# Kernel tuning notes

Hardware: AMD Instinct MI355X
Metric: run time of the kernel (lower is better)

Reference implementation:

```python
import jax, jax.numpy as jnp
import numpy as np

ALPHA = 1.5
EPS = 1e-5
N_BISECT = 30

BSZ, NFIELD, NFEAT, NEMB, DK, NHID, MLP_NHID, NOUT = 2048, 100, 100000, 64, 64, 256, 1024, 1


def _entmax_bisect(x):
    """alpha-entmax (alpha=1.5) along last axis via bisection on tau."""
    x = x * (ALPHA - 1.0)
    mx = jnp.max(x, axis=-1, keepdims=True)
    d = x.shape[-1]
    tau_lo = mx - 1.0
    tau_hi = mx - (1.0 / d) ** (ALPHA - 1.0)
    inv_am1 = 1.0 / (ALPHA - 1.0)  # = 2.0 for alpha=1.5

    def p_of(tau):
        return jnp.maximum(x - tau, 0.0) ** inv_am1

    dm0 = tau_hi - tau_lo

    def body(i, carry):
        tau_lo, dm = carry
        dm = dm * 0.5
        tau_m = tau_lo + dm
        f_m = jnp.sum(p_of(tau_m), axis=-1, keepdims=True) - 1.0
        tau_lo = jnp.where(f_m >= 0, tau_m, tau_lo)
        return (tau_lo, dm)

    tau_lo, dm = jax.lax.fori_loop(0, N_BISECT, body, (tau_lo, dm0))
    p = p_of(tau_lo)
    return p / jnp.sum(p, axis=-1, keepdims=True)


@jax.custom_vjp
def entmax(x):
    return _entmax_bisect(x)

def _entmax_fwd(x):
    p = _entmax_bisect(x)
    return p, p

def _entmax_bwd(p, g):
    # exact entmax jacobian-vector product (as in entmax library)
    gppr = jnp.where(p > 0, p ** (2.0 - ALPHA), 0.0)
    dx = g * gppr
    q = jnp.sum(dx, axis=-1, keepdims=True) / jnp.sum(gppr, axis=-1, keepdims=True)
    return (dx - q * gppr,)

entmax.defvjp(_entmax_fwd, _entmax_bwd)


def _bn(x, gamma, beta, axes, ch_shape):
    mean = jnp.mean(x, axis=axes, keepdims=True)
    var = jnp.var(x, axis=axes, keepdims=True)
    return gamma.reshape(ch_shape) * (x - mean) / jnp.sqrt(var + EPS) + beta.reshape(ch_shape)


def setup_inputs() -> dict:
    key = jax.random.key(0)
    ks = jax.random.split(key, 12)
    inp = {
        "ids": jax.random.randint(ks[0], (BSZ, NFIELD), 0, NFEAT),
        "values": jax.random.uniform(ks[1], (BSZ, NFIELD), dtype=jnp.float32),
        "emb_table": jax.random.normal(ks[2], (NFEAT, NEMB), dtype=jnp.float32) * 0.01,
        "w_bilinear": jax.random.normal(ks[3], (DK, NEMB), dtype=jnp.float32) * (1.0 / np.sqrt(NEMB)),
        "query": jax.random.normal(ks[4], (NHID, DK), dtype=jnp.float32) * (1.414 / np.sqrt(NHID + DK)),
        "att_values": jax.random.normal(ks[5], (NHID, NFIELD), dtype=jnp.float32) * 0.01,
        "bn_gamma": jnp.ones((NHID,), jnp.float32),
        "bn_beta": jnp.zeros((NHID,), jnp.float32),
        "mlp_w0": jax.random.normal(ks[6], (MLP_NHID, NHID * NEMB), dtype=jnp.float32) * (1.0 / np.sqrt(NHID * NEMB)),
        "mlp_b0": jnp.zeros((MLP_NHID,), jnp.float32),
        "mlp_g0": jnp.ones((MLP_NHID,), jnp.float32),
        "mlp_be0": jnp.zeros((MLP_NHID,), jnp.float32),
        "mlp_w1": jax.random.normal(ks[7], (MLP_NHID, MLP_NHID), dtype=jnp.float32) * (1.0 / np.sqrt(MLP_NHID)),
        "mlp_b1": jnp.zeros((MLP_NHID,), jnp.float32),
        "mlp_g1": jnp.ones((MLP_NHID,), jnp.float32),
        "mlp_be1": jnp.zeros((MLP_NHID,), jnp.float32),
        "out_w": jax.random.normal(ks[8], (NOUT, MLP_NHID), dtype=jnp.float32) * (1.0 / np.sqrt(MLP_NHID)),
        "out_b": jnp.zeros((NOUT,), jnp.float32),
    }
    return inp


def reference(ids, values, emb_table, w_bilinear, query, att_values, bn_gamma, bn_beta,
              mlp_w0, mlp_b0, mlp_g0, mlp_be0, mlp_w1, mlp_b1, mlp_g1, mlp_be1, out_w, out_b):
    v = jnp.clip(values, 0.001, 1.0)                        # [b,f]
    emb = emb_table[ids] * v[..., None]                     # [b,f,e]
    keys = jnp.einsum('bfe,ke->bfk', emb, w_bilinear)       # [b,f,dk]
    gates = jnp.einsum('bfk,ok->bof', keys, query) * (DK ** -0.5)  # [b,o,f]
    sparse_gates = entmax(gates)                            # [b,o,f]
    arm_w = sparse_gates * att_values[None]                 # [b,o,f]
    arm = jnp.exp(jnp.einsum('bfe,bof->boe', emb, arm_w))   # [b,o,e]
    arm = _bn(arm, bn_gamma, bn_beta, axes=(0, 2), ch_shape=(1, -1, 1))
    h = arm.reshape(arm.shape[0], -1)                       # [b, o*e]
    h = jax.nn.relu(_bn(h @ mlp_w0.T + mlp_b0, mlp_g0, mlp_be0, axes=(0,), ch_shape=(1, -1)))
    h = jax.nn.relu(_bn(h @ mlp_w1.T + mlp_b1, mlp_g1, mlp_be1, axes=(0,), ch_shape=(1, -1)))
    y = h @ out_w.T + out_b                                 # [b,1]
    return y.squeeze(-1)
```

## Files before the change

kernel.cpp:

```cpp
#include <hip/hip_runtime.h>

typedef unsigned short u16;
typedef __attribute__((ext_vector_type(8))) short bf16x8;
typedef __attribute__((ext_vector_type(8))) unsigned short u16x8;
typedef __attribute__((ext_vector_type(4))) float f32x4;

__device__ __forceinline__ u16 f2bf(float f) {
  unsigned u = __builtin_bit_cast(unsigned, f);
  u += 0x7fffu + ((u >> 16) & 1u);
  return (u16)(u >> 16);
}
__device__ __forceinline__ float bf2f(u16 h) {
  unsigned u = ((unsigned)h) << 16;
  return __builtin_bit_cast(float, u);
}

#define NB 2048
#define NF 100
#define NE 64
#define NO 256
#define OCH 64
#define EMB_ST 72
#define EMBT_ST 136
#define GAW_ST 136

#define GLOAD16(gsrc, ldst)                                                        \
  __builtin_amdgcn_global_load_lds(                                                \
      (const __attribute__((address_space(1))) unsigned int*)(gsrc),               \
      (__attribute__((address_space(3))) unsigned int*)(ldst), 16, 0, 0)

__global__ void k_prep(const float* __restrict__ wb, const float* __restrict__ q,
                       u16* __restrict__ mt, const float* __restrict__ w1,
                       u16* __restrict__ w1bf) {
  if (blockIdx.x < 64) {
    int idx = blockIdx.x * 256 + threadIdx.x;
    int o = idx >> 6, e = idx & 63;
    float s = 0.f;
    for (int k = 0; k < 64; ++k) s = fmaf(q[o * 64 + k], wb[k * 64 + e], s);
    mt[idx] = f2bf(s * 0.0625f);
  } else {
    int i4 = ((blockIdx.x - 64) * 256 + threadIdx.x) * 4;
    float4 v = *(const float4*)(w1 + i4);
    ushort4 o;
    o.x = f2bf(v.x); o.y = f2bf(v.y); o.z = f2bf(v.z); o.w = f2bf(v.w);
    *(ushort4*)(w1bf + i4) = o;
  }
}

__global__ void k_cvt_w0s(const float* __restrict__ in, const float* __restrict__ scl,
                          u16* __restrict__ out) {
  size_t i4 = ((size_t)blockIdx.x * 256 + threadIdx.x) * 4;
  int o = (int)((i4 >> 6) & 255);
  float sc = scl[o];
  float4 v = *(const float4*)(in + i4);
  ushort4 u;
  u.x = f2bf(v.x * sc); u.y = f2bf(v.y * sc);
  u.z = f2bf(v.z * sc); u.w = f2bf(v.w * sc);
  *(ushort4*)(out + i4) = u;
}

__global__ __launch_bounds__(256) void k_mega(
    const int* __restrict__ ids, const float* __restrict__ vals,
    const float* __restrict__ etab, const u16* __restrict__ mt,
    const float* __restrict__ att, u16* __restrict__ tbuf,
    float* __restrict__ pstatB) {
  __shared__ u16 s_emb[112][EMB_ST];
  __shared__ u16 s_embT[64][EMBT_ST];
  __shared__ u16 s_gaw[64][GAW_ST];
  __shared__ float s_rs[64];
  __shared__ float s_ps[256][2];

  const int tid = threadIdx.x;
  const int lane = tid & 63;
  const int wid = tid >> 6;
  const int b = blockIdx.x;

  for (int f = wid; f < NF; f += 4) {
    int id = ids[b * NF + f];
    float v = vals[b * NF + f];
    v = fminf(fmaxf(v, 0.001f), 1.0f);
    float ev = etab[(size_t)id * NE + lane] * v;
    u16 bf = f2bf(ev);
    s_emb[f][lane] = bf;
    s_embT[lane][f] = bf;
  }
  for (int i = tid; i < 12 * EMB_ST; i += 256) s_emb[100 + i / EMB_ST][i % EMB_ST] = 0;
  for (int i = tid; i < 64 * 36; i += 256) s_embT[i / 36][100 + i % 36] = 0;
  for (int i = tid; i < 64 * 24; i += 256) s_gaw[i / 24][112 + i % 24] = 0;
  __syncthreads();

  for (int oc = 0; oc < 4; ++oc) {
    const int obase = oc * OCH;
    bf16x8 amt[2];
#pragma unroll
    for (int kh = 0; kh < 2; ++kh)
      amt[kh] = *(const bf16x8*)(mt + ((obase + wid * 16 + (lane & 15)) * 64 +
                                       kh * 32 + ((lane >> 4) * 8)));

#pragma unroll
    for (int ft = 0; ft < 7; ++ft) {
      f32x4 acc = {0.f, 0.f, 0.f, 0.f};
#pragma unroll
      for (int kh = 0; kh < 2; ++kh) {
        bf16x8 bfr = *(const bf16x8*)&s_emb[ft * 16 + (lane & 15)][kh * 32 + ((lane >> 4) * 8)];
        acc = __builtin_amdgcn_mfma_f32_16x16x32_bf16(amt[kh], bfr, acc, 0, 0, 0);
      }
      int fc = ft * 16 + (lane & 15);
      if (fc < NF) {
#pragma unroll
        for (int i = 0; i < 4; ++i)
          s_gaw[wid * 16 + ((lane >> 4) * 4) + i][fc] = f2bf(acc[i]);
      }
    }
    asm volatile("" ::: "memory");

    {
      const int q = lane & 3;
      const int rl = lane >> 2;
      const int r = wid * 16 + rl;
      const int og = obase + r;
      float x[28];
#pragma unroll
      for (int j = 0; j < 7; ++j) {
        ushort4 g = *(const ushort4*)&s_gaw[r][j * 16 + q * 4];
        x[j * 4 + 0] = bf2f(g.x); x[j * 4 + 1] = bf2f(g.y);
        x[j * 4 + 2] = bf2f(g.z); x[j * 4 + 3] = bf2f(g.w);
      }
      if (q > 0) { x[24] = -1e30f; x[25] = -1e30f; x[26] = -1e30f; x[27] = -1e30f; }
      float attv[28];
#pragma unroll
      for (int j = 0; j < 7; ++j) {
        if (j < 6 || q == 0) {
          float4 av = *(const float4*)(att + og * NF + j * 16 + q * 4);
          attv[j * 4 + 0] = av.x; attv[j * 4 + 1] = av.y;
          attv[j * 4 + 2] = av.z; attv[j * 4 + 3] = av.w;
        } else {
          attv[j * 4 + 0] = 0.f; attv[j * 4 + 1] = 0.f;
          attv[j * 4 + 2] = 0.f; attv[j * 4 + 3] = 0.f;
        }
      }
      float m0 = x[0], m1 = x[1];
#pragma unroll
      for (int j = 2; j < 28; j += 2) { m0 = fmaxf(m0, x[j]); m1 = fmaxf(m1, x[j + 1]); }
      float mx = fmaxf(m0, m1);
      mx = fmaxf(mx, __shfl_xor(mx, 1));
      mx = fmaxf(mx, __shfl_xor(mx, 2));
      float tau = mx - 1.0f;
#pragma unroll
      for (int it = 0; it < 5; ++it) {
        float s0 = 0.f, s1 = 0.f, t0 = 0.f, t1 = 0.f;
#pragma unroll
        for (int j = 0; j < 14; ++j) {
          float d0 = fmaxf(x[j] - tau, 0.f);
          float d1 = fmaxf(x[j + 14] - tau, 0.f);
          s0 = fmaf(d0, d0, s0); s1 = fmaf(d1, d1, s1);
          t0 += d0; t1 += d1;
        }
        float s = s0 + s1, sd = t0 + t1;
        s += __shfl_xor(s, 1);
        s += __shfl_xor(s, 2);
        sd += __shfl_xor(sd, 1);
        sd += __shfl_xor(sd, 2);
        float den = 2.0f * sd + 1e-30f;
        float inv;
        asm("v_rcp_f32 %0, %1" : "=v"(inv) : "v"(den));
        tau += (s - 1.0f) * inv;
      }
      float s0 = 0.f, s1 = 0.f;
#pragma unroll
      for (int j = 0; j < 14; ++j) {
        float d0 = fmaxf(x[j] - tau, 0.f);
        float d1 = fmaxf(x[j + 14] - tau, 0.f);
        x[j] = d0 * d0;
        x[j + 14] = d1 * d1;
        s0 += x[j]; s1 += x[j + 14];
      }
      float s = s0 + s1;
      s += __shfl_xor(s, 1);
      s += __shfl_xor(s, 2);
      if (q == 0) s_rs[r] = 1.0f / s;
#pragma unroll
      for (int j = 0; j < 7; ++j) {
        ushort4 w;
        w.x = f2bf(x[j * 4 + 0] * attv[j * 4 + 0]);
        w.y = f2bf(x[j * 4 + 1] * attv[j * 4 + 1]);
        w.z = f2bf(x[j * 4 + 2] * attv[j * 4 + 2]);
        w.w = f2bf(x[j * 4 + 3] * attv[j * 4 + 3]);
        *(ushort4*)&s_gaw[r][j * 16 + q * 4] = w;
      }
    }
    asm volatile("" ::: "memory");

    f32x4 acc[4] = {};
#pragma unroll
    for (int h = 0; h < 4; ++h) {
      bf16x8 afr = *(const bf16x8*)&s_gaw[wid * 16 + (lane & 15)][h * 32 + ((lane >> 4) * 8)];
#pragma unroll
      for (int et = 0; et < 4; ++et) {
        bf16x8 bfr = *(const bf16x8*)&s_embT[et * 16 + (lane & 15)][h * 32 + ((lane >> 4) * 8)];
        acc[et] = __builtin_amdgcn_mfma_f32_16x16x32_bf16(afr, bfr, acc[et], 0, 0, 0);
      }
    }
    const int rloc = wid * 16 + ((lane >> 4) * 4);
    float rs4[4];
#pragma unroll
    for (int i = 0; i < 4; ++i) rs4[i] = s_rs[rloc + i];
    float tval[4][4];
#pragma unroll
    for (int et = 0; et < 4; ++et)
#pragma unroll
      for (int i = 0; i < 4; ++i)
        tval[et][i] = __expf(acc[et][i] * rs4[i]) - 1.0f;
    size_t orow = (size_t)b * NO + obase + rloc;
#pragma unroll
    for (int et = 0; et < 4; ++et) {
      int e = et * 16 + (lane & 15);
#pragma unroll
      for (int i = 0; i < 4; ++i)
        tbuf[(orow + i) * 64 + e] = f2bf(tval[et][i]);
    }
#pragma unroll
    for (int i = 0; i < 4; ++i) {
      float sp = tval[0][i] + tval[1][i] + tval[2][i] + tval[3][i];
      float sq = fmaf(tval[0][i], tval[0][i],
                 fmaf(tval[1][i], tval[1][i],
                 fmaf(tval[2][i], tval[2][i], tval[3][i] * tval[3][i])));
#pragma unroll
      for (int m = 1; m < 16; m <<= 1) {
        sp += __shfl_xor(sp, m);
        sq += __shfl_xor(sq, m);
      }
      if ((lane & 15) == 0) {
        s_ps[obase + rloc + i][0] = sp;
        s_ps[obase + rloc + i][1] = sq;
      }
    }
    asm volatile("" ::: "memory");
  }
  __syncthreads();
  *(float2*)&pstatB[(size_t)b * 512 + tid * 2] =
      make_float2(s_ps[tid][0], s_ps[tid][1]);
}

__global__ void k_stats_o_fin2(const float* __restrict__ pstatB,
                               const float* __restrict__ g, float* __restrict__ scl) {
  const int o = blockIdx.x;
  float s = 0.f, s2 = 0.f;
  for (int bb = threadIdx.x; bb < NB; bb += 256) {
    float2 v = *(const float2*)&pstatB[(size_t)bb * 512 + o * 2];
    s += v.x; s2 += v.y;
  }
  __shared__ float red[2][256];
  red[0][threadIdx.x] = s; red[1][threadIdx.x] = s2;
  __syncthreads();
  for (int st = 128; st >= 1; st >>= 1) {
    if (threadIdx.x < st) {
      red[0][threadIdx.x] += red[0][threadIdx.x + st];
      red[1][threadIdx.x] += red[1][threadIdx.x + st];
    }
    __syncthreads();
  }
  if (threadIdx.x == 0) {
    float invN = 1.0f / (float)(NB * 64);
    float m = red[0][0] * invN;
    float var = red[1][0] * invN - m * m;
    scl[o] = g[o] * rsqrtf(var + 1e-5f);
  }
}

__global__ __launch_bounds__(256) void k_gemmp(const u16* __restrict__ A,
                                               const u16* __restrict__ B,
                                               float* __restrict__ C,
                                               int M, int N, int K, int ksz) {
  __shared__ u16 lds[4 * 8192];
  const int tid = threadIdx.x, lane = tid & 63, wid = tid >> 6;
  const int wr = wid >> 1, wc = wid & 1;

  const int nx = gridDim.x, ny = gridDim.y;
  const int nwg = nx * ny * gridDim.z;
  int lin = blockIdx.x + nx * (blockIdx.y + ny * blockIdx.z);
  int swz = (lin & 7) * (nwg >> 3) + (lin >> 3);
  const int bx = swz % nx;
  const int byz = swz / nx;
  const int by = byz % ny, bz = byz / ny;

  const int m0 = bx * 128, n0 = by * 128;
  const int k0 = bz * ksz;
  C += (size_t)bz * ((size_t)M * N);

  f32x4 acc[4][4];
#pragma unroll
  for (int mi = 0; mi < 4; ++mi)
#pragma unroll
    for (int ni = 0; ni < 4; ++ni) acc[mi][ni] = (f32x4){0.f, 0.f, 0.f, 0.f};

  const int gchunk = (lane & 3) ^ ((lane >> 3) & 3);
  const u16* gstage = (wid < 2)
      ? A + (size_t)(m0 + wid * 64 + (lane >> 2)) * K + k0 + gchunk * 8
      : B + (size_t)(n0 + (wid - 2) * 64 + (lane >> 2)) * K + k0 + gchunk * 8;
  const int lstage = (wid < 2) ? (wid * 64) * 32 : 4096 + ((wid - 2) * 64) * 32;

  const int la15 = lane & 15, la4 = lane >> 4;
  int aoffs[4], boffs[4];
#pragma unroll
  for (int i = 0; i < 4; ++i) {
    int ra = wr * 64 + i * 16 + la15;
    aoffs[i] = ra * 32 + ((la4 ^ ((ra >> 1) & 3)) * 8);
    int rb = wc * 64 + i * 16 + la15;
    boffs[i] = 4096 + rb * 32 + ((la4 ^ ((rb >> 1) & 3)) * 8);
  }

  const int nkt = ksz / 32;
#pragma unroll
  for (int t = 0; t < 4; ++t)
#pragma unroll
    for (int i = 0; i < 4; ++i)
      GLOAD16(gstage + (size_t)t * 32 + (size_t)i * 16 * K, lds + t * 8192 + lstage + i * 512);
  asm volatile("s_waitcnt vmcnt(8)" ::: "memory");
  __builtin_amdgcn_sched_barrier(0);
  __builtin_amdgcn_s_barrier();
  __builtin_amdgcn_sched_barrier(0);

  int pbase = 0;
  for (int jj = 0; jj < nkt; jj += 2) {
    const int sa = pbase, sb = pbase + 8192;
    bf16x8 af0[4], bf0[4], af1[4], bf1[4];
#pragma unroll
    for (int i = 0; i < 4; ++i) {
      af0[i] = *(const bf16x8*)(lds + sa + aoffs[i]);
      bf0[i] = *(const bf16x8*)(lds + sa + boffs[i]);
      af1[i] = *(const bf16x8*)(lds + sb + aoffs[i]);
      bf1[i] = *(const bf16x8*)(lds + sb + boffs[i]);
    }
    asm volatile("s_waitcnt lgkmcnt(0)" ::: "memory");
    __builtin_amdgcn_sched_barrier(0);
    __builtin_amdgcn_s_barrier();
    __builtin_amdgcn_sched_barrier(0);
    const int ts0 = (jj + 4 < nkt) ? jj + 4 : nkt - 1;
    const int ts1 = (jj + 5 < nkt) ? jj + 5 : nkt - 1;
#pragma unroll
    for (int i = 0; i < 4; ++i)
      GLOAD16(gstage + (size_t)ts0 * 32 + (size_t)i * 16 * K, lds + sa + lstage + i * 512);
#pragma unroll
    for (int i = 0; i < 4; ++i)
      GLOAD16(gstage + (size_t)ts1 * 32 + (size_t)i * 16 * K, lds + sb + lstage + i * 512);
    __builtin_amdgcn_s_setprio(1);
#pragma unroll
    for (int mi = 0; mi < 4; ++mi)
#pragma unroll
      for (int ni = 0; ni < 4; ++ni)
        acc[mi][ni] = __builtin_amdgcn_mfma_f32_16x16x32_bf16(af0[mi], bf0[ni], acc[mi][ni], 0, 0, 0);
#pragma unroll
    for (int mi = 0; mi < 4; ++mi)
#pragma unroll
      for (int ni = 0; ni < 4; ++ni)
        acc[mi][ni] = __builtin_amdgcn_mfma_f32_16x16x32_bf16(af1[mi], bf1[ni], acc[mi][ni], 0, 0, 0);
    __builtin_amdgcn_s_setprio(0);
    asm volatile("s_waitcnt vmcnt(8)" ::: "memory");
    __builtin_amdgcn_sched_barrier(0);
    __builtin_amdgcn_s_barrier();
    __builtin_amdgcn_sched_barrier(0);
    pbase ^= 16384;
  }

#pragma unroll
  for (int mi = 0; mi < 4; ++mi) {
    int m = m0 + wr * 64 + mi * 16 + ((lane >> 4) * 4);
#pragma unroll
    for (int ni = 0; ni < 4; ++ni) {
      int n = n0 + wc * 64 + ni * 16 + (lane & 15);
#pragma unroll
      for (int i = 0; i < 4; ++i) C[(size_t)(m + i) * N + n] = acc[mi][ni][i];
    }
  }
}

template <int NP>
__global__ void k_red_stats(const float* __restrict__ c, float* __restrict__ r,
                            float* __restrict__ pstat) {
  const int col = blockIdx.x * 64 + (threadIdx.x & 63);
  const int rt = threadIdx.x >> 6;
  const int rg = blockIdx.y;
  const size_t ps = (size_t)NB * 1024;
  float s = 0.f, s2 = 0.f;
  for (int rr = rt; rr < 64; rr += 4) {
    size_t idx = (size_t)(rg * 64 + rr) * 1024 + col;
    float v = c[idx];
#pragma unroll
    for (int p = 1; p < NP; ++p) v += c[p * ps + idx];
    r[idx] = v;
    s += v;
    s2 = fmaf(v, v, s2);
  }
  __shared__ float red[2][256];
  red[0][threadIdx.x] = s; red[1][threadIdx.x] = s2;
  __syncthreads();
  if (threadIdx.x < 64) {
    int t = threadIdx.x;
    s  = red[0][t] + red[0][t + 64] + red[0][t + 128] + red[0][t + 192];
    s2 = red[1][t] + red[1][t + 64] + red[1][t + 128] + red[1][t + 192];
    pstat[((size_t)rg * 1024 + col) * 2]     = s;
    pstat[((size_t)rg * 1024 + col) * 2 + 1] = s2;
  }
}

__global__ void k_stats_fin(const float* __restrict__ pstat,
                            const float* __restrict__ g, const float* __restrict__ be,
                            float* __restrict__ scl, float* __restrict__ bia) {
  int col = blockIdx.x * 256 + threadIdx.x;
  float s = 0.f, s2 = 0.f;
#pragma unroll
  for (int p = 0; p < 32; ++p) {
    s  += pstat[((size_t)p * 1024 + col) * 2];
    s2 += pstat[((size_t)p * 1024 + col) * 2 + 1];
  }
  float invN = 1.0f / (float)NB;
  float m = s * invN;
  float var = s2 * invN - m * m;
  float inv = rsqrtf(var + 1e-5f);
  scl[col] = g[col] * inv;
  bia[col] = be[col] - g[col] * inv * m;
}

__global__ void k_applyA1(const float* __restrict__ c0,
                          const float* __restrict__ scl, const float* __restrict__ bia,
                          u16* __restrict__ a1) {
  size_t i4 = ((size_t)blockIdx.x * 256 + threadIdx.x) * 4;
  int n = (int)(i4 & 1023);
  float4 v0 = *(const float4*)(c0 + i4);
  ushort4 o;
  o.x = f2bf(fmaxf(fmaf(v0.x, scl[n + 0], bia[n + 0]), 0.f));
  o.y = f2bf(fmaxf(fmaf(v0.y, scl[n + 1], bia[n + 1]), 0.f));
  o.z = f2bf(fmaxf(fmaf(v0.z, scl[n + 2], bia[n + 2]), 0.f));
  o.w = f2bf(fmaxf(fmaf(v0.w, scl[n + 3], bia[n + 3]), 0.f));
  *(ushort4*)(a1 + i4) = o;
}

__global__ void k_final(const float* __restrict__ h, const float* __restrict__ scl,
                        const float* __restrict__ bia, const float* __restrict__ ow,
                        const float* __restrict__ ob, float* __restrict__ y) {
  int lane = threadIdx.x & 63, wid = threadIdx.x >> 6;
  int row = blockIdx.x * 4 + wid;
  const float* hr = h + (size_t)row * 1024;
  float part = 0.f;
#pragma unroll
  for (int j = 0; j < 16; ++j) {
    int n = j * 64 + lane;
    float v = fmaxf(fmaf(hr[n], scl[n], bia[n]), 0.f);
    part = fmaf(v, ow[n], part);
  }
#pragma unroll
  for (int off = 32; off >= 1; off >>= 1) part += __shfl_xor(part, off);
  if (lane == 0) y[row] = part + ob[0];
}

extern "C" void kernel_launch(void* const* d_in, const int* in_sizes, int n_in,
                              void* d_out, int out_size, void* d_ws, size_t ws_size,
                              hipStream_t stream) {
  const int*   ids   = (const int*)d_in[0];
  const float* vals  = (const float*)d_in[1];
  const float* etab  = (const float*)d_in[2];
  const float* wb    = (const float*)d_in[3];
  const float* query = (const float*)d_in[4];
  const float* att   = (const float*)d_in[5];
  const float* bng   = (const float*)d_in[6];
  const float* w0    = (const float*)d_in[8];
  const float* g0    = (const float*)d_in[10];
  const float* be0   = (const float*)d_in[11];
  const float* w1    = (const float*)d_in[12];
  const float* g1    = (const float*)d_in[14];
  const float* be1   = (const float*)d_in[15];
  const float* outw  = (const float*)d_in[16];
  const float* outb  = (const float*)d_in[17];
  float* y = (float*)d_out;

  char* ws = (char*)d_ws;
  u16*   mt     = (u16*)(ws + 0);
  u16*   w0bf   = (u16*)(ws + 32768ull);
  u16*   w1bf   = (u16*)(ws + 33587200ull);
  u16*   tbuf   = (u16*)(ws + 35684352ull);
  float* c01    = (float*)(ws + 102793216ull);
  float* h1     = (float*)(ws + 102793216ull);
  float* r0     = (float*)(ws + 169902080ull);
  u16*   a1     = (u16*)(ws + 178290688ull);
  float* pstatB = (float*)(ws + 182484992ull);
  float* h      = (float*)(ws + 186679296ull);
  float* pstat1 = (float*)(ws + 195067904ull);
  float* pstat2 = (float*)(ws + 195330048ull);
  float* sclA   = (float*)(ws + 195608576ull);
  float* scl1   = (float*)(ws + 195609600ull);
  float* bia1   = (float*)(ws + 195613696ull);
  float* scl2   = (float*)(ws + 195617792ull);
  float* bia2   = (float*)(ws + 195621888ull);

  k_prep<<<1088, 256, 0, stream>>>(wb, query, mt, w1, w1bf);
  k_mega<<<2048, 256, 0, stream>>>(ids, vals, etab, mt, att, tbuf, pstatB);
  k_stats_o_fin2<<<256, 256, 0, stream>>>(pstatB, bng, sclA);
  k_cvt_w0s<<<16384, 256, 0, stream>>>(w0, sclA, w0bf);
  k_gemmp<<<dim3(16, 8, 4), 256, 0, stream>>>(tbuf, w0bf, c01, 2048, 1024, 16384, 4096);
  k_red_stats<4><<<dim3(16, 32), 256, 0, stream>>>(c01, r0, pstat1);
  k_stats_fin<<<4, 256, 0, stream>>>(pstat1, g0, be0, scl1, bia1);
  k_applyA1<<<2048, 256, 0, stream>>>(r0, scl1, bia1, a1);
  k_gemmp<<<dim3(16, 8, 4), 256, 0, stream>>>(a1, w1bf, h1, 2048, 1024, 1024, 256);
  k_red_stats<4><<<dim3(16, 32), 256, 0, stream>>>(h1, h, pstat2);
  k_stats_fin<<<4, 256, 0, stream>>>(pstat2, g1, be1, scl2, bia2);
  k_final<<<512, 256, 0, stream>>>(h, scl2, bia2, outw, outb, y);
}
```

Measured before the change: 253.0 us.

## Add 128x256-tile triple-buffered GEMM with split-K 8 for first MLP layer

Introduces a new bf16 MFMA GEMM kernel that uses a 128x256 output tile per workgroup and a three-stage LDS ring of async global loads, with barriers and priority hints around the MFMA block. The first MLP GEMM now uses this kernel with split-K raised from 4 to 8, keeping the workgroup count the same. The reduction kernel is switched to sum 8 partials. The larger tile is meant to improve operand reuse and hide load latency. The cost is twice as much partial-sum traffic written and read back in the reduction step.

Result: no change. 255.5 us (+1.0%).

```diff
diff --git a/kernel.cpp b/kernel.cpp
--- a/kernel.cpp
+++ b/kernel.cpp
@@ -265,6 +265,112 @@
     float m = red[0][0] * invN;
     float var = red[1][0] * invN - m * m;
     scl[o] = g[o] * rsqrtf(var + 1e-5f);
+  }
+}
+
+__global__ __launch_bounds__(256, 2) void k_gemmw(const u16* __restrict__ A,
+                                                  const u16* __restrict__ B,
+                                                  float* __restrict__ C,
+                                                  int M, int N, int K, int ksz) {
+  __shared__ u16 lds[3 * 12288];
+  const int tid = threadIdx.x, lane = tid & 63, wid = tid >> 6;
+  const int wr = wid >> 1, wc = wid & 1;
+
+  const int nx = gridDim.x, ny = gridDim.y;
+  const int nwg = nx * ny * gridDim.z;
+  int lin = blockIdx.x + nx * (blockIdx.y + ny * blockIdx.z);
+  int swz = (lin & 7) * (nwg >> 3) + (lin >> 3);
+  const int bx = swz % nx;
+  const int byz = swz / nx;
+  const int by = byz % ny, bz = byz / ny;
+
+  const int m0 = bx * 128, n0 = by * 256;
+  const int k0 = bz * ksz;
+  C += (size_t)bz * ((size_t)M * N);
+
+  f32x4 acc[4][8];
+#pragma unroll
+  for (int mi = 0; mi < 4; ++mi)
+#pragma unroll
+    for (int ni = 0; ni < 8; ++ni) acc[mi][ni] = (f32x4){0.f, 0.f, 0.f, 0.f};
+
+  const int gchunk = (lane & 3) ^ ((lane >> 3) & 3);
+  const u16* gsrc[6];
+  int ldst[6];
+#pragma unroll
+  for (int s = 0; s < 6; ++s) {
+    int u = wid * 6 + s;
+    if (u < 8) {
+      gsrc[s] = A + (size_t)(m0 + u * 16 + (lane >> 2)) * K + k0 + gchunk * 8;
+      ldst[s] = u * 512;
+    } else {
+      gsrc[s] = B + (size_t)(n0 + (u - 8) * 16 + (lane >> 2)) * K + k0 + gchunk * 8;
+      ldst[s] = 4096 + (u - 8) * 512;
+    }
+  }
+
+  const int la15 = lane & 15, la4 = lane >> 4;
+  int aoffs[4], boffs[8];
+#pragma unroll
+  for (int i = 0; i < 4; ++i) {
+    int ra = wr * 64 + i * 16 + la15;
+    aoffs[i] = ra * 32 + ((la4 ^ ((ra >> 1) & 3)) * 8);
+  }
+#pragma unroll
+  for (int j = 0; j < 8; ++j) {
+    int rb = wc * 128 + j * 16 + la15;
+    boffs[j] = 4096 + rb * 32 + ((la4 ^ ((rb >> 1) & 3)) * 8);
+  }
+
+  const int nkt = ksz / 32;
+#pragma unroll
+  for (int t = 0; t < 3; ++t)
+#pragma unroll
+    for (int s = 0; s < 6; ++s)
+      GLOAD16(gsrc[s] + (size_t)t * 32, lds + t * 12288 + ldst[s]);
+  asm volatile("s_waitcnt vmcnt(12)" ::: "memory");
+  __builtin_amdgcn_sched_barrier(0);
+  __builtin_amdgcn_s_barrier();
+  __builtin_amdgcn_sched_barrier(0);
+
+  int slot = 0;
+  for (int j = 0; j < nkt; ++j) {
+    bf16x8 af[4], bfv[8];
+#pragma unroll
+    for (int i = 0; i < 4; ++i) af[i] = *(const bf16x8*)(lds + slot * 12288 + aoffs[i]);
+#pragma unroll
+    for (int i = 0; i < 8; ++i) bfv[i] = *(const bf16x8*)(lds + slot * 12288 + boffs[i]);
+    asm volatile("s_waitcnt lgkmcnt(0)" ::: "memory");
+    __builtin_amdgcn_sched_barrier(0);
+    __builtin_amdgcn_s_barrier();
+    __builtin_amdgcn_sched_barrier(0);
+    const int ts = (j + 3 < nkt) ? j + 3 : nkt - 1;
+#pragma unroll
+    for (int s = 0; s < 6; ++s)
+      GLOAD16(gsrc[s] + (size_t)ts * 32, lds + slot * 12288 + ldst[s]);
+    __builtin_amdgcn_s_setprio(1);
+#pragma unroll
+    for (int mi = 0; mi < 4; ++mi)
+#pragma unroll
+      for (int ni = 0; ni < 8; ++ni)
+        acc[mi][ni] = __builtin_amdgcn_mfma_f32_16x16x32_bf16(af[mi], bfv[ni], acc[mi][ni], 0, 0, 0);
+    __builtin_amdgcn_s_setprio(0);
+    asm volatile("s_waitcnt vmcnt(12)" ::: "memory");
+    __builtin_amdgcn_sched_barrier(0);
+    __builtin_amdgcn_s_barrier();
+    __builtin_amdgcn_sched_barrier(0);
+    slot = (slot == 2) ? 0 : slot + 1;
+  }
+
+#pragma unroll
+  for (int mi = 0; mi < 4; ++mi) {
+    int m = m0 + wr * 64 + mi * 16 + ((lane >> 4) * 4);
+#pragma unroll
+    for (int ni = 0; ni < 8; ++ni) {
+      int n = n0 + wc * 128 + ni * 16 + (lane & 15);
+#pragma unroll
+      for (int i = 0; i < 4; ++i) C[(size_t)(m + i) * N + n] = acc[mi][ni][i];
+    }
   }
 }
 
@@ -497,8 +603,8 @@
   k_mega<<<2048, 256, 0, stream>>>(ids, vals, etab, mt, att, tbuf, pstatB);
   k_stats_o_fin2<<<256, 256, 0, stream>>>(pstatB, bng, sclA);
   k_cvt_w0s<<<16384, 256, 0, stream>>>(w0, sclA, w0bf);
-  k_gemmp<<<dim3(16, 8, 4), 256, 0, stream>>>(tbuf, w0bf, c01, 2048, 1024, 16384, 4096);
-  k_red_stats<4><<<dim3(16, 32), 256, 0, stream>>>(c01, r0, pstat1);
+  k_gemmw<<<dim3(16, 4, 8), 256, 0, stream>>>(tbuf, w0bf, c01, 2048, 1024, 16384, 2048);
+  k_red_stats<8><<<dim3(16, 32), 256, 0, stream>>>(c01, r0, pstat1);
   k_stats_fin<<<4, 256, 0, stream>>>(pstat1, g0, be0, scl1, bia1);
   k_applyA1<<<2048, 256, 0, stream>>>(r0, scl1, bia1, a1);
   k_gemmp<<<dim3(16, 8, 4), 256, 0, stream>>>(a1, w1bf, h1, 2048, 1024, 1024, 256);
```
